# Kernel tuning notes

Hardware: AMD Instinct MI355X
Metric: run time of the kernel (lower is better)

## Reference

```python
import jax, jax.numpy as jnp
import numpy as np
import math

D = 768
H = 12
DFF = 3072
HD = D // H


def _layernorm(x, g, b, eps=1e-5):
    mu = jnp.mean(x, axis=-1, keepdims=True)
    var = jnp.var(x, axis=-1, keepdims=True)
    return (x - mu) * jax.lax.rsqrt(var + eps) * g + b


def setup_inputs() -> dict:
    key = jax.random.key(0)
    ks = jax.random.split(key, 12)
    B, S = 2, 4096
    s = 1.0 / math.sqrt(D)
    sf = 1.0 / math.sqrt(DFF)
    return {
        "x": jax.random.normal(ks[0], (B, S, D), jnp.float32),
        "attention_mask": jnp.ones((B, S), jnp.int32),
        "ln1_g": jnp.ones((D,), jnp.float32),
        "ln1_b": jnp.zeros((D,), jnp.float32),
        "ln2_g": jnp.ones((D,), jnp.float32),
        "ln2_b": jnp.zeros((D,), jnp.float32),
        "Wq": jax.random.normal(ks[1], (D, D), jnp.float32) * s,
        "bq": jnp.zeros((D,), jnp.float32),
        "Wk": jax.random.normal(ks[2], (D, D), jnp.float32) * s,
        "bk": jnp.zeros((D,), jnp.float32),
        "Wv": jax.random.normal(ks[3], (D, D), jnp.float32) * s,
        "bv": jnp.zeros((D,), jnp.float32),
        "Wo": jax.random.normal(ks[4], (D, D), jnp.float32) * s,
        "bo": jnp.zeros((D,), jnp.float32),
        "W1": jax.random.normal(ks[5], (D, DFF), jnp.float32) * s,
        "b1": jnp.zeros((DFF,), jnp.float32),
        "W2": jax.random.normal(ks[6], (DFF, D), jnp.float32) * sf,
        "b2": jnp.zeros((D,), jnp.float32),
    }


def _block(x, attention_mask, ln1_g, ln1_b, ln2_g, ln2_b,
           Wq, bq, Wk, bk, Wv, bv, Wo, bo, W1, b1, W2, b2):
    B, S, _ = x.shape
    h = _layernorm(x, ln1_g, ln1_b)
    q = (h @ Wq + bq).reshape(B, S, H, HD)
    k = (h @ Wk + bk).reshape(B, S, H, HD)
    v = (h @ Wv + bv).reshape(B, S, H, HD)
    # scores: [B, H, S, S]
    dots = jnp.einsum('bqhd,bkhd->bhqk', q, k) / math.sqrt(HD)
    causal = jnp.tril(jnp.ones((S, S), bool))  # True = keep
    keep = causal[None, None] & (attention_mask != 0)[:, None, None, :]
    dots = jnp.where(keep, dots, -jnp.inf)
    probs = jax.nn.softmax(dots, axis=-1)
    ctx = jnp.einsum('bhqk,bkhd->bqhd', probs, v).reshape(B, S, D)
    sa = ctx @ Wo + bo  # dropout = identity (eval)
    x = x + sa
    h2 = _layernorm(x, ln2_g, ln2_b)
    ff = jax.nn.relu(h2 @ W1 + b1) @ W2 + b2
    return x + ff


def reference(x, attention_mask, ln1_g, ln1_b, ln2_g, ln2_b,
              Wq, bq, Wk, bk, Wv, bv, Wo, bo, W1, b1, W2, b2):
    return _block(x, attention_mask, ln1_g, ln1_b, ln2_g, ln2_b,
                  Wq, bq, Wk, bk, Wv, bv, Wo, bo, W1, b1, W2, b2)
```

## Files before the change

### kernel.cpp

```cpp
#include <hip/hip_runtime.h>
#include <hip/hip_bf16.h>
#include <math.h>

#define S_LEN 4096
#define DMODEL 768
#define NHEAD 12
#define HDIM 64
#define DFF_ 3072
#define MROWS 8192

typedef __bf16 bf16;
typedef __bf16 bf16x4 __attribute__((ext_vector_type(4)));
typedef __bf16 bf16x8 __attribute__((ext_vector_type(8)));
typedef float f32x4 __attribute__((ext_vector_type(4)));

union F4 { float4 v; float f[4]; };
union U2 { bf16 h[2]; unsigned u; };
union U8 { unsigned u[4]; bf16x8 v; };

__device__ __forceinline__ void gld_lds16(void* lds, const void* g) {
    __builtin_amdgcn_global_load_lds(
        (const __attribute__((address_space(1))) unsigned int*)g,
        (__attribute__((address_space(3))) unsigned int*)lds, 16, 0, 0);
}

template<typename OUT>
__global__ __launch_bounds__(256) void ln_kernel(const float* __restrict__ x,
                                                 const float* __restrict__ g,
                                                 const float* __restrict__ bta,
                                                 OUT* __restrict__ out) {
    const int row = blockIdx.x;
    const int t = threadIdx.x;
    const float* xr = x + (size_t)row * DMODEL;
    float v0 = xr[t], v1 = xr[t + 256], v2 = xr[t + 512];
    float s = v0 + v1 + v2;
    float ss = v0 * v0 + v1 * v1 + v2 * v2;
    for (int o = 32; o > 0; o >>= 1) {
        s += __shfl_down(s, o, 64);
        ss += __shfl_down(ss, o, 64);
    }
    __shared__ float sm[4], sm2[4];
    const int w = t >> 6, lane = t & 63;
    if (lane == 0) { sm[w] = s; sm2[w] = ss; }
    __syncthreads();
    s = sm[0] + sm[1] + sm[2] + sm[3];
    ss = sm2[0] + sm2[1] + sm2[2] + sm2[3];
    const float mu = s * (1.0f / DMODEL);
    const float var = ss * (1.0f / DMODEL) - mu * mu;
    const float rs = rsqrtf(var + 1e-5f);
    OUT* orow = out + (size_t)row * DMODEL;
    orow[t]       = (OUT)((v0 - mu) * rs * g[t]       + bta[t]);
    orow[t + 256] = (OUT)((v1 - mu) * rs * g[t + 256] + bta[t + 256]);
    orow[t + 512] = (OUT)((v2 - mu) * rs * g[t + 512] + bta[t + 512]);
}

__global__ __launch_bounds__(256) void wtrans_kernel(const float* __restrict__ W,
                                                     bf16* __restrict__ Wt,
                                                     int K, int N) {
    __shared__ float tile[64][65];
    const int tid = threadIdx.x;
    const int n0 = blockIdx.x * 64, k0 = blockIdx.y * 64;
    const int lr = tid >> 4, lc = (tid & 15) << 2;
#pragma unroll
    for (int i = 0; i < 4; ++i) {
        const int r = lr + i * 16;
        F4 w; w.v = *(const float4*)&W[(size_t)(k0 + r) * N + n0 + lc];
#pragma unroll
        for (int j = 0; j < 4; ++j) tile[r][lc + j] = w.f[j];
    }
    __syncthreads();
#pragma unroll
    for (int i = 0; i < 4; ++i) {
        const int n = lr + i * 16;
        bf16x4 o;
#pragma unroll
        for (int j = 0; j < 4; ++j) o[j] = (bf16)tile[lc + j][n];
        *(bf16x4*)&Wt[(size_t)(n0 + n) * K + k0 + lc] = o;
    }
}

template<bool RELU, bool RES, bool OUT_BF16>
__global__ __launch_bounds__(256) void mgemm_kernel(
    const bf16* __restrict__ A,
    const bf16* __restrict__ Wt0, const float* __restrict__ bias0, void* __restrict__ C0,
    const bf16* __restrict__ Wt1, const float* __restrict__ bias1, void* __restrict__ C1,
    const bf16* __restrict__ Wt2, const float* __restrict__ bias2, void* __restrict__ C2,
    const float* __restrict__ R, int M, int N, int K,
    float sc0, float sc1, float sc2) {
    const bf16* Wt = Wt0; const float* bias = bias0; void* C = C0; float sc = sc0;
    if (blockIdx.z == 1) { Wt = Wt1; bias = bias1; C = C1; sc = sc1; }
    if (blockIdx.z == 2) { Wt = Wt2; bias = bias2; C = C2; sc = sc2; }

    __shared__ bf16 As[128 * 32];
    __shared__ bf16 Bs[128 * 32];

    const int tid = threadIdx.x;
    const int wave = tid >> 6, lane = tid & 63;
    const int row0 = blockIdx.y * 128, col0 = blockIdx.x * 128;
    const int wr = (wave >> 1) * 64, wc = (wave & 1) * 64;
    const int mrow = lane & 15, kq = (lane >> 4) * 8;

    const int st_row = (lane >> 2);
    const int st_off = (lane & 3) * 16;

    f32x4 acc[4][4] = {};

    const char* Ab = (const char*)(A + (size_t)row0 * K);
    const char* Bb = (const char*)(Wt + (size_t)col0 * K);
    const size_t strideA = (size_t)K * 2;

    for (int k0 = 0; k0 < K; k0 += 32) {
#pragma unroll
        for (int issue = 0; issue < 2; ++issue) {
            const int r = wave * 32 + issue * 16 + st_row;
            gld_lds16((char*)As + (wave * 32 + issue * 16) * 64,
                      Ab + (size_t)r * strideA + k0 * 2 + st_off);
            gld_lds16((char*)Bs + (wave * 32 + issue * 16) * 64,
                      Bb + (size_t)r * strideA + k0 * 2 + st_off);
        }
        __syncthreads();
        bf16x8 af[4], bfr[4];
#pragma unroll
        for (int mi = 0; mi < 4; ++mi)
            af[mi] = *(const bf16x8*)&As[(wr + mi * 16 + mrow) * 32 + kq];
#pragma unroll
        for (int ni = 0; ni < 4; ++ni)
            bfr[ni] = *(const bf16x8*)&Bs[(wc + ni * 16 + mrow) * 32 + kq];
#pragma unroll
        for (int mi = 0; mi < 4; ++mi)
#pragma unroll
            for (int ni = 0; ni < 4; ++ni)
                acc[mi][ni] = __builtin_amdgcn_mfma_f32_16x16x32_bf16(
                    af[mi], bfr[ni], acc[mi][ni], 0, 0, 0);
        __syncthreads();
    }

    const int quad = lane >> 4;
    float bv[4];
#pragma unroll
    for (int ni = 0; ni < 4; ++ni) bv[ni] = bias[col0 + wc + ni * 16 + mrow];
#pragma unroll
    for (int mi = 0; mi < 4; ++mi) {
#pragma unroll
        for (int r = 0; r < 4; ++r) {
            const int row = row0 + wr + mi * 16 + quad * 4 + r;
#pragma unroll
            for (int ni = 0; ni < 4; ++ni) {
                const int col = col0 + wc + ni * 16 + mrow;
                float v = acc[mi][ni][r] + bv[ni];
                if (RES) v += R[(size_t)row * N + col];
                v *= sc;
                if (RELU) v = fmaxf(v, 0.0f);
                if (OUT_BF16) ((bf16*)C)[(size_t)row * N + col] = (bf16)v;
                else          ((float*)C)[(size_t)row * N + col] = v;
            }
        }
    }
}

__global__ __launch_bounds__(256) void mattn_kernel(
    const bf16* __restrict__ Q, const bf16* __restrict__ K,
    const bf16* __restrict__ V, const int* __restrict__ amask,
    bf16* __restrict__ O) {
    const int bx = blockIdx.x, h = blockIdx.y, b = blockIdx.z;

    __shared__ bf16 Ks[64][72];
    __shared__ bf16 Vt[64][72];
    __shared__ bf16 Os[64][72];
    __shared__ float mk[64];
    __shared__ int flagv;

    const int tid = threadIdx.x;
    const int wave = tid >> 6, lane = tid & 63;
    const int l = lane & 15, quad = lane >> 4;
    const int qh = quad >> 1;
    const int srcA = (quad & 1) * 32 + l;
    const int srcB = srcA + 16;
    const float NEG_INF = -__builtin_huge_valf();

    const int kr = tid >> 2, ks = (tid & 3) * 16;
    const int vk0 = (tid & 31) * 2, vds = (tid >> 5) * 8;

#pragma unroll 1
    for (int pass = 0; pass < 2; ++pass) {
        const int qt = pass ? bx : (63 - bx);

        const bf16* Qb = Q + (size_t)(b * S_LEN + qt * 64 + wave * 16 + l) * DMODEL + h * HDIM;
        const bf16x8 qf0 = *(const bf16x8*)(Qb + quad * 8);
        const bf16x8 qf1 = *(const bf16x8*)(Qb + 32 + quad * 8);

        float m_run = NEG_INF, l_run = 0.0f;
        f32x4 acc[4] = {};

        for (int kt = 0; kt <= qt; ++kt) {
            __syncthreads();
            {
                const bf16* kg = K + (size_t)(b * S_LEN + kt * 64 + kr) * DMODEL + h * HDIM + ks;
                *(bf16x8*)&Ks[kr][ks]     = *(const bf16x8*)kg;
                *(bf16x8*)&Ks[kr][ks + 8] = *(const bf16x8*)(kg + 8);
            }
            {
                const bf16* vg = V + (size_t)(b * S_LEN + kt * 64 + vk0) * DMODEL + h * HDIM + vds;
                bf16x8 v0 = *(const bf16x8*)vg;
                bf16x8 v1 = *(const bf16x8*)(vg + DMODEL);
#pragma unroll
                for (int i = 0; i < 8; ++i) {
                    U2 w; w.h[0] = v0[i]; w.h[1] = v1[i];
                    *(unsigned*)&Vt[vds + i][vk0] = w.u;
                }
            }
            if (wave == 0) {
                const int mv = amask[b * S_LEN + kt * 64 + lane];
                mk[lane] = mv ? 0.0f : NEG_INF;
                unsigned long long bal = __ballot(mv != 0);
                if (lane == 0) flagv = (bal == ~0ULL);
            }
            __syncthreads();
            const int allv = flagv;

            f32x4 sreg[4] = {};
#pragma unroll
            for (int mi = 0; mi < 4; ++mi) {
                bf16x8 kf0 = *(const bf16x8*)&Ks[mi * 16 + l][quad * 8];
                bf16x8 kf1 = *(const bf16x8*)&Ks[mi * 16 + l][32 + quad * 8];
                sreg[mi] = __builtin_amdgcn_mfma_f32_16x16x32_bf16(kf0, qf0, sreg[mi], 0, 0, 0);
                sreg[mi] = __builtin_amdgcn_mfma_f32_16x16x32_bf16(kf1, qf1, sreg[mi], 0, 0, 0);
            }
            if (!allv) {
#pragma unroll
                for (int mi = 0; mi < 4; ++mi) {
                    F4 m4; m4.v = *(const float4*)&mk[mi * 16 + quad * 4];
#pragma unroll
                    for (int r = 0; r < 4; ++r) sreg[mi][r] += m4.f[r];
                }
            }
            if (kt == qt) {
#pragma unroll
                for (int mi = 0; mi < 4; ++mi)
#pragma unroll
                    for (int r = 0; r < 4; ++r)
                        if (mi * 16 + quad * 4 + r > wave * 16 + l)
                            sreg[mi][r] = NEG_INF;
            }

            float mloc = sreg[0][0];
#pragma unroll
            for (int mi = 0; mi < 4; ++mi)
#pragma unroll
                for (int r = 0; r < 4; ++r) mloc = fmaxf(mloc, sreg[mi][r]);
            mloc = fmaxf(mloc, __shfl_xor(mloc, 16, 64));
            mloc = fmaxf(mloc, __shfl_xor(mloc, 32, 64));
            const float mn = fmaxf(m_run, mloc);
            const float alpha = __builtin_amdgcn_exp2f(m_run - mn);
            m_run = mn;
            float ls = 0.0f;
#pragma unroll
            for (int mi = 0; mi < 4; ++mi)
#pragma unroll
                for (int r = 0; r < 4; ++r) {
                    const float p = __builtin_amdgcn_exp2f(sreg[mi][r] - mn);
                    sreg[mi][r] = p;
                    ls += p;
                }
            ls += __shfl_xor(ls, 16, 64);
            ls += __shfl_xor(ls, 32, 64);
            l_run = l_run * alpha + ls;
#pragma unroll
            for (int mi = 0; mi < 4; ++mi)
#pragma unroll
                for (int r = 0; r < 4; ++r) acc[mi][r] *= alpha;

            unsigned pk[4][2];
#pragma unroll
            for (int mi = 0; mi < 4; ++mi) {
                U2 w0; w0.h[0] = (bf16)sreg[mi][0]; w0.h[1] = (bf16)sreg[mi][1];
                U2 w1; w1.h[0] = (bf16)sreg[mi][2]; w1.h[1] = (bf16)sreg[mi][3];
                pk[mi][0] = w0.u; pk[mi][1] = w1.u;
            }
            bf16x8 pfrag[2];
#pragma unroll
            for (int kc = 0; kc < 2; ++kc) {
                U8 u;
#pragma unroll
                for (int t = 0; t < 2; ++t) {
                    const unsigned a0 = (unsigned)__shfl((int)pk[2 * kc][t],     srcA, 64);
                    const unsigned b0 = (unsigned)__shfl((int)pk[2 * kc + 1][t], srcA, 64);
                    u.u[t] = qh ? b0 : a0;
                    const unsigned a1 = (unsigned)__shfl((int)pk[2 * kc][t],     srcB, 64);
                    const unsigned b1 = (unsigned)__shfl((int)pk[2 * kc + 1][t], srcB, 64);
                    u.u[2 + t] = qh ? b1 : a1;
                }
                pfrag[kc] = u.v;
            }
#pragma unroll
            for (int mi = 0; mi < 4; ++mi) {
                bf16x8 vf0 = *(const bf16x8*)&Vt[mi * 16 + l][quad * 8];
                bf16x8 vf1 = *(const bf16x8*)&Vt[mi * 16 + l][32 + quad * 8];
                acc[mi] = __builtin_amdgcn_mfma_f32_16x16x32_bf16(vf0, pfrag[0], acc[mi], 0, 0, 0);
                acc[mi] = __builtin_amdgcn_mfma_f32_16x16x32_bf16(vf1, pfrag[1], acc[mi], 0, 0, 0);
            }
        }

        const float rinv = 1.0f / l_run;
#pragma unroll
        for (int mi = 0; mi < 4; ++mi) {
            U2 w0; w0.h[0] = (bf16)(acc[mi][0] * rinv); w0.h[1] = (bf16)(acc[mi][1] * rinv);
            U2 w1; w1.h[0] = (bf16)(acc[mi][2] * rinv); w1.h[1] = (bf16)(acc[mi][3] * rinv);
            *(unsigned*)&Os[wave * 16 + l][mi * 16 + quad * 4]     = w0.u;
            *(unsigned*)&Os[wave * 16 + l][mi * 16 + quad * 4 + 2] = w1.u;
        }
        __syncthreads();
        {
            const int orow = tid >> 2, oseg = (tid & 3) * 16;
            bf16* Og = O + (size_t)(b * S_LEN + qt * 64 + orow) * DMODEL + h * HDIM + oseg;
            *(bf16x8*)Og       = *(const bf16x8*)&Os[orow][oseg];
            *(bf16x8*)(Og + 8) = *(const bf16x8*)&Os[orow][oseg + 8];
        }
    }
}

extern "C" void kernel_launch(void* const* d_in, const int* in_sizes, int n_in,
                              void* d_out, int out_size, void* d_ws, size_t ws_size,
                              hipStream_t stream) {
    const float* x     = (const float*)d_in[0];
    const int*   amask = (const int*)  d_in[1];
    const float* ln1_g = (const float*)d_in[2];
    const float* ln1_b = (const float*)d_in[3];
    const float* ln2_g = (const float*)d_in[4];
    const float* ln2_b = (const float*)d_in[5];
    const float* Wq = (const float*)d_in[6];  const float* bq = (const float*)d_in[7];
    const float* Wk = (const float*)d_in[8];  const float* bk = (const float*)d_in[9];
    const float* Wv = (const float*)d_in[10]; const float* bv = (const float*)d_in[11];
    const float* Wo = (const float*)d_in[12]; const float* bo = (const float*)d_in[13];
    const float* W1 = (const float*)d_in[14]; const float* b1 = (const float*)d_in[15];
    const float* W2 = (const float*)d_in[16]; const float* b2 = (const float*)d_in[17];
    float* out = (float*)d_out;

    char* ws = (char*)d_ws;
    const size_t WSML = (size_t)DMODEL * DMODEL * 2;
    const size_t WBIG = (size_t)DMODEL * DFF_ * 2;
    bf16* Wqt = (bf16*)(ws + 0 * WSML);
    bf16* Wkt = (bf16*)(ws + 1 * WSML);
    bf16* Wvt = (bf16*)(ws + 2 * WSML);
    bf16* Wot = (bf16*)(ws + 3 * WSML);
    bf16* W1t = (bf16*)(ws + 4 * WSML);
    bf16* W2t = (bf16*)(ws + 4 * WSML + WBIG);
    char* act = ws + 4 * WSML + 2 * WBIG;

    const size_t HB = (size_t)MROWS * DMODEL * 2;
    const size_t FB = (size_t)MROWS * DMODEL * 4;
    bf16*  h    = (bf16*)(act);
    bf16*  qb   = (bf16*)(act + HB);
    bf16*  kb   = (bf16*)(act + 2 * HB);
    bf16*  vb   = (bf16*)(act + 3 * HB);
    bf16*  ctx  = h;
    float* x1   = (float*)(act + 4 * HB);
    bf16*  f    = (bf16*)(act + 4 * HB + FB);
    bf16*  h2   = h;

    const float SCL = 0.125f * 1.44269504089f;

    wtrans_kernel<<<dim3(DMODEL / 64, DMODEL / 64), 256, 0, stream>>>(Wq, Wqt, DMODEL, DMODEL);
    wtrans_kernel<<<dim3(DMODEL / 64, DMODEL / 64), 256, 0, stream>>>(Wk, Wkt, DMODEL, DMODEL);
    wtrans_kernel<<<dim3(DMODEL / 64, DMODEL / 64), 256, 0, stream>>>(Wv, Wvt, DMODEL, DMODEL);
    wtrans_kernel<<<dim3(DMODEL / 64, DMODEL / 64), 256, 0, stream>>>(Wo, Wot, DMODEL, DMODEL);
    wtrans_kernel<<<dim3(DFF_ / 64, DMODEL / 64), 256, 0, stream>>>(W1, W1t, DMODEL, DFF_);
    wtrans_kernel<<<dim3(DMODEL / 64, DFF_ / 64), 256, 0, stream>>>(W2, W2t, DFF_, DMODEL);

    ln_kernel<bf16><<<MROWS, 256, 0, stream>>>(x, ln1_g, ln1_b, h);
    mgemm_kernel<false, false, true><<<dim3(DMODEL / 128, MROWS / 128, 3), 256, 0, stream>>>(
        h, Wqt, bq, qb, Wkt, bk, kb, Wvt, bv, vb, nullptr, MROWS, DMODEL, DMODEL,
        SCL, 1.0f, 1.0f);
    mattn_kernel<<<dim3(32, NHEAD, 2), 256, 0, stream>>>(qb, kb, vb, amask, ctx);
    mgemm_kernel<false, true, false><<<dim3(DMODEL / 128, MROWS / 128, 1), 256, 0, stream>>>(
        ctx, Wot, bo, x1, Wot, bo, x1, Wot, bo, x1, x, MROWS, DMODEL, DMODEL,
        1.0f, 1.0f, 1.0f);
    ln_kernel<bf16><<<MROWS, 256, 0, stream>>>(x1, ln2_g, ln2_b, h2);
    mgemm_kernel<true, false, true><<<dim3(DFF_ / 128, MROWS / 128, 1), 256, 0, stream>>>(
        h2, W1t, b1, f, W1t, b1, f, W1t, b1, f, nullptr, MROWS, DFF_, DMODEL,
        1.0f, 1.0f, 1.0f);
    mgemm_kernel<false, true, false><<<dim3(DMODEL / 128, MROWS / 128, 1), 256, 0, stream>>>(
        f, W2t, b2, out, W2t, b2, out, W2t, b2, out, x1, MROWS, DMODEL, DFF_,
        1.0f, 1.0f, 1.0f);
}
```

Before: 515.0 us.

## Use 64-row GEMM tiles for N=768 GEMMs and one query tile per attention block

The GEMM kernel gains an MT template parameter. The output-projection and FFN-down GEMMs (N=768) now use 64x128 tiles, which doubles their block count and should fill the GPU better. The attention kernel drops its paired-pass scheme and gives each block a single query tile over a 64-wide grid, heaviest tiles first, so there are more blocks to schedule. LDS padding shrinks from 72 to 68 columns, which can change bank-conflict behaviour. The trade-off is lower per-block reuse of the B tiles in the smaller GEMMs and possibly worse load balance in attention.

```diff
diff --git a/kernel.cpp b/kernel.cpp
--- a/kernel.cpp
+++ b/kernel.cpp
@@ -79,7 +79,7 @@
     }
 }
 
-template<bool RELU, bool RES, bool OUT_BF16>
+template<int MT, bool RELU, bool RES, bool OUT_BF16>
 __global__ __launch_bounds__(256) void mgemm_kernel(
     const bf16* __restrict__ A,
     const bf16* __restrict__ Wt0, const float* __restrict__ bias0, void* __restrict__ C0,
@@ -91,61 +91,73 @@
     if (blockIdx.z == 1) { Wt = Wt1; bias = bias1; C = C1; sc = sc1; }
     if (blockIdx.z == 2) { Wt = Wt2; bias = bias2; C = C2; sc = sc2; }
 
-    __shared__ bf16 As[128 * 32];
+    constexpr int NI = (MT == 128) ? 4 : 2;
+    __shared__ bf16 As[MT * 32];
     __shared__ bf16 Bs[128 * 32];
 
     const int tid = threadIdx.x;
     const int wave = tid >> 6, lane = tid & 63;
-    const int row0 = blockIdx.y * 128, col0 = blockIdx.x * 128;
-    const int wr = (wave >> 1) * 64, wc = (wave & 1) * 64;
+    const int row0 = blockIdx.y * MT, col0 = blockIdx.x * 128;
+    const int wr = (MT == 128) ? (wave >> 1) * 64 : 0;
+    const int wc = (MT == 128) ? (wave & 1) * 64 : wave * 32;
     const int mrow = lane & 15, kq = (lane >> 4) * 8;
 
     const int st_row = (lane >> 2);
     const int st_off = (lane & 3) * 16;
 
-    f32x4 acc[4][4] = {};
+    f32x4 acc[4][NI] = {};
 
     const char* Ab = (const char*)(A + (size_t)row0 * K);
     const char* Bb = (const char*)(Wt + (size_t)col0 * K);
     const size_t strideA = (size_t)K * 2;
 
     for (int k0 = 0; k0 < K; k0 += 32) {
+        if (MT == 128) {
+#pragma unroll
+            for (int issue = 0; issue < 2; ++issue) {
+                const int r = wave * 32 + issue * 16 + st_row;
+                gld_lds16((char*)As + (wave * 32 + issue * 16) * 64,
+                          Ab + (size_t)r * strideA + k0 * 2 + st_off);
+            }
+        } else {
+            const int r = wave * 16 + st_row;
+            gld_lds16((char*)As + (wave * 16) * 64,
+                      Ab + (size_t)r * strideA + k0 * 2 + st_off);
+        }
 #pragma unroll
         for (int issue = 0; issue < 2; ++issue) {
             const int r = wave * 32 + issue * 16 + st_row;
-            gld_lds16((char*)As + (wave * 32 + issue * 16) * 64,
-                      Ab + (size_t)r * strideA + k0 * 2 + st_off);
             gld_lds16((char*)Bs + (wave * 32 + issue * 16) * 64,
                       Bb + (size_t)r * strideA + k0 * 2 + st_off);
         }
         __syncthreads();
-        bf16x8 af[4], bfr[4];
+        bf16x8 af[4], bfr[NI];
 #pragma unroll
         for (int mi = 0; mi < 4; ++mi)
             af[mi] = *(const bf16x8*)&As[(wr + mi * 16 + mrow) * 32 + kq];
 #pragma unroll
-        for (int ni = 0; ni < 4; ++ni)
+        for (int ni = 0; ni < NI; ++ni)
             bfr[ni] = *(const bf16x8*)&Bs[(wc + ni * 16 + mrow) * 32 + kq];
 #pragma unroll
         for (int mi = 0; mi < 4; ++mi)
 #pragma unroll
-            for (int ni = 0; ni < 4; ++ni)
+            for (int ni = 0; ni < NI; ++ni)
                 acc[mi][ni] = __builtin_amdgcn_mfma_f32_16x16x32_bf16(
                     af[mi], bfr[ni], acc[mi][ni], 0, 0, 0);
         __syncthreads();
     }
 
     const int quad = lane >> 4;
-    float bv[4];
-#pragma unroll
-    for (int ni = 0; ni < 4; ++ni) bv[ni] = bias[col0 + wc + ni * 16 + mrow];
+    float bv[NI];
+#pragma unroll
+    for (int ni = 0; ni < NI; ++ni) bv[ni] = bias[col0 + wc + ni * 16 + mrow];
 #pragma unroll
     for (int mi = 0; mi < 4; ++mi) {
 #pragma unroll
         for (int r = 0; r < 4; ++r) {
             const int row = row0 + wr + mi * 16 + quad * 4 + r;
 #pragma unroll
-            for (int ni = 0; ni < 4; ++ni) {
+            for (int ni = 0; ni < NI; ++ni) {
                 const int col = col0 + wc + ni * 16 + mrow;
                 float v = acc[mi][ni][r] + bv[ni];
                 if (RES) v += R[(size_t)row * N + col];
@@ -162,11 +174,12 @@
     const bf16* __restrict__ Q, const bf16* __restrict__ K,
     const bf16* __restrict__ V, const int* __restrict__ amask,
     bf16* __restrict__ O) {
-    const int bx = blockIdx.x, h = blockIdx.y, b = blockIdx.z;
-
-    __shared__ bf16 Ks[64][72];
-    __shared__ bf16 Vt[64][72];
-    __shared__ bf16 Os[64][72];
+    const int qt = 63 - blockIdx.x;
+    const int h = blockIdx.y, b = blockIdx.z;
+
+    __shared__ bf16 Ks[64][68];
+    __shared__ bf16 Vt[64][68];
+    __shared__ bf16 Os[64][68];
     __shared__ float mk[64];
     __shared__ int flagv;
 
@@ -181,141 +194,136 @@
     const int kr = tid >> 2, ks = (tid & 3) * 16;
     const int vk0 = (tid & 31) * 2, vds = (tid >> 5) * 8;
 
-#pragma unroll 1
-    for (int pass = 0; pass < 2; ++pass) {
-        const int qt = pass ? bx : (63 - bx);
-
-        const bf16* Qb = Q + (size_t)(b * S_LEN + qt * 64 + wave * 16 + l) * DMODEL + h * HDIM;
-        const bf16x8 qf0 = *(const bf16x8*)(Qb + quad * 8);
-        const bf16x8 qf1 = *(const bf16x8*)(Qb + 32 + quad * 8);
-
-        float m_run = NEG_INF, l_run = 0.0f;
-        f32x4 acc[4] = {};
-
-        for (int kt = 0; kt <= qt; ++kt) {
-            __syncthreads();
-            {
-                const bf16* kg = K + (size_t)(b * S_LEN + kt * 64 + kr) * DMODEL + h * HDIM + ks;
-                *(bf16x8*)&Ks[kr][ks]     = *(const bf16x8*)kg;
-                *(bf16x8*)&Ks[kr][ks + 8] = *(const bf16x8*)(kg + 8);
-            }
-            {
-                const bf16* vg = V + (size_t)(b * S_LEN + kt * 64 + vk0) * DMODEL + h * HDIM + vds;
-                bf16x8 v0 = *(const bf16x8*)vg;
-                bf16x8 v1 = *(const bf16x8*)(vg + DMODEL);
-#pragma unroll
-                for (int i = 0; i < 8; ++i) {
-                    U2 w; w.h[0] = v0[i]; w.h[1] = v1[i];
-                    *(unsigned*)&Vt[vds + i][vk0] = w.u;
-                }
-            }
-            if (wave == 0) {
-                const int mv = amask[b * S_LEN + kt * 64 + lane];
-                mk[lane] = mv ? 0.0f : NEG_INF;
-                unsigned long long bal = __ballot(mv != 0);
-                if (lane == 0) flagv = (bal == ~0ULL);
-            }
-            __syncthreads();
-            const int allv = flagv;
-
-            f32x4 sreg[4] = {};
-#pragma unroll
-            for (int mi = 0; mi < 4; ++mi) {
-                bf16x8 kf0 = *(const bf16x8*)&Ks[mi * 16 + l][quad * 8];
-                bf16x8 kf1 = *(const bf16x8*)&Ks[mi * 16 + l][32 + quad * 8];
-                sreg[mi] = __builtin_amdgcn_mfma_f32_16x16x32_bf16(kf0, qf0, sreg[mi], 0, 0, 0);
-                sreg[mi] = __builtin_amdgcn_mfma_f32_16x16x32_bf16(kf1, qf1, sreg[mi], 0, 0, 0);
-            }
-            if (!allv) {
-#pragma unroll
-                for (int mi = 0; mi < 4; ++mi) {
-                    F4 m4; m4.v = *(const float4*)&mk[mi * 16 + quad * 4];
-#pragma unroll
-                    for (int r = 0; r < 4; ++r) sreg[mi][r] += m4.f[r];
-                }
-            }
-            if (kt == qt) {
-#pragma unroll
-                for (int mi = 0; mi < 4; ++mi)
-#pragma unroll
-                    for (int r = 0; r < 4; ++r)
-                        if (mi * 16 + quad * 4 + r > wave * 16 + l)
-                            sreg[mi][r] = NEG_INF;
-            }
-
-            float mloc = sreg[0][0];
-#pragma unroll
-            for (int mi = 0; mi < 4; ++mi)
-#pragma unroll
-                for (int r = 0; r < 4; ++r) mloc = fmaxf(mloc, sreg[mi][r]);
-            mloc = fmaxf(mloc, __shfl_xor(mloc, 16, 64));
-            mloc = fmaxf(mloc, __shfl_xor(mloc, 32, 64));
-            const float mn = fmaxf(m_run, mloc);
-            const float alpha = __builtin_amdgcn_exp2f(m_run - mn);
-            m_run = mn;
-            float ls = 0.0f;
-#pragma unroll
-            for (int mi = 0; mi < 4; ++mi)
-#pragma unroll
-                for (int r = 0; r < 4; ++r) {
-                    const float p = __builtin_amdgcn_exp2f(sreg[mi][r] - mn);
-                    sreg[mi][r] = p;
-                    ls += p;
-                }
-            ls += __shfl_xor(ls, 16, 64);
-            ls += __shfl_xor(ls, 32, 64);
-            l_run = l_run * alpha + ls;
-#pragma unroll
-            for (int mi = 0; mi < 4; ++mi)
-#pragma unroll
-                for (int r = 0; r < 4; ++r) acc[mi][r] *= alpha;
-
-            unsigned pk[4][2];
-#pragma unroll
-            for (int mi = 0; mi < 4; ++mi) {
-                U2 w0; w0.h[0] = (bf16)sreg[mi][0]; w0.h[1] = (bf16)sreg[mi][1];
-                U2 w1; w1.h[0] = (bf16)sreg[mi][2]; w1.h[1] = (bf16)sreg[mi][3];
-                pk[mi][0] = w0.u; pk[mi][1] = w1.u;
-            }
-            bf16x8 pfrag[2];
-#pragma unroll
-            for (int kc = 0; kc < 2; ++kc) {
-                U8 u;
-#pragma unroll
-                for (int t = 0; t < 2; ++t) {
-                    const unsigned a0 = (unsigned)__shfl((int)pk[2 * kc][t],     srcA, 64);
-                    const unsigned b0 = (unsigned)__shfl((int)pk[2 * kc + 1][t], srcA, 64);
-                    u.u[t] = qh ? b0 : a0;
-                    const unsigned a1 = (unsigned)__shfl((int)pk[2 * kc][t],     srcB, 64);
-                    const unsigned b1 = (unsigned)__shfl((int)pk[2 * kc + 1][t], srcB, 64);
-                    u.u[2 + t] = qh ? b1 : a1;
-                }
-                pfrag[kc] = u.v;
-            }
-#pragma unroll
-            for (int mi = 0; mi < 4; ++mi) {
-                bf16x8 vf0 = *(const bf16x8*)&Vt[mi * 16 + l][quad * 8];
-                bf16x8 vf1 = *(const bf16x8*)&Vt[mi * 16 + l][32 + quad * 8];
-                acc[mi] = __builtin_amdgcn_mfma_f32_16x16x32_bf16(vf0, pfrag[0], acc[mi], 0, 0, 0);
-                acc[mi] = __builtin_amdgcn_mfma_f32_16x16x32_bf16(vf1, pfrag[1], acc[mi], 0, 0, 0);
-            }
-        }
-
-        const float rinv = 1.0f / l_run;
-#pragma unroll
-        for (int mi = 0; mi < 4; ++mi) {
-            U2 w0; w0.h[0] = (bf16)(acc[mi][0] * rinv); w0.h[1] = (bf16)(acc[mi][1] * rinv);
-            U2 w1; w1.h[0] = (bf16)(acc[mi][2] * rinv); w1.h[1] = (bf16)(acc[mi][3] * rinv);
-            *(unsigned*)&Os[wave * 16 + l][mi * 16 + quad * 4]     = w0.u;
-            *(unsigned*)&Os[wave * 16 + l][mi * 16 + quad * 4 + 2] = w1.u;
-        }
+    const bf16* Qb = Q + (size_t)(b * S_LEN + qt * 64 + wave * 16 + l) * DMODEL + h * HDIM;
+    const bf16x8 qf0 = *(const bf16x8*)(Qb + quad * 8);
+    const bf16x8 qf1 = *(const bf16x8*)(Qb + 32 + quad * 8);
+
+    float m_run = NEG_INF, l_run = 0.0f;
+    f32x4 acc[4] = {};
+
+    for (int kt = 0; kt <= qt; ++kt) {
         __syncthreads();
         {
-            const int orow = tid >> 2, oseg = (tid & 3) * 16;
-            bf16* Og = O + (size_t)(b * S_LEN + qt * 64 + orow) * DMODEL + h * HDIM + oseg;
-            *(bf16x8*)Og       = *(const bf16x8*)&Os[orow][oseg];
-            *(bf16x8*)(Og + 8) = *(const bf16x8*)&Os[orow][oseg + 8];
-        }
+            const bf16* kg = K + (size_t)(b * S_LEN + kt * 64 + kr) * DMODEL + h * HDIM + ks;
+            *(bf16x8*)&Ks[kr][ks]     = *(const bf16x8*)kg;
+            *(bf16x8*)&Ks[kr][ks + 8] = *(const bf16x8*)(kg + 8);
+        }
+        {
+            const bf16* vg = V + (size_t)(b * S_LEN + kt * 64 + vk0) * DMODEL + h * HDIM + vds;
+            bf16x8 v0 = *(const bf16x8*)vg;
+            bf16x8 v1 = *(const bf16x8*)(vg + DMODEL);
+#pragma unroll
+            for (int i = 0; i < 8; ++i) {
+                U2 w; w.h[0] = v0[i]; w.h[1] = v1[i];
+                *(unsigned*)&Vt[vds + i][vk0] = w.u;
+            }
+        }
+        if (wave == 0) {
+            const int mv = amask[b * S_LEN + kt * 64 + lane];
+            mk[lane] = mv ? 0.0f : NEG_INF;
+            unsigned long long bal = __ballot(mv != 0);
+            if (lane == 0) flagv = (bal == ~0ULL);
+        }
+        __syncthreads();
+        const int allv = flagv;
+
+        f32x4 sreg[4] = {};
+#pragma unroll
+        for (int mi = 0; mi < 4; ++mi) {
+            bf16x8 kf0 = *(const bf16x8*)&Ks[mi * 16 + l][quad * 8];
+            bf16x8 kf1 = *(const bf16x8*)&Ks[mi * 16 + l][32 + quad * 8];
+            sreg[mi] = __builtin_amdgcn_mfma_f32_16x16x32_bf16(kf0, qf0, sreg[mi], 0, 0, 0);
+            sreg[mi] = __builtin_amdgcn_mfma_f32_16x16x32_bf16(kf1, qf1, sreg[mi], 0, 0, 0);
+        }
+        if (!allv) {
+#pragma unroll
+            for (int mi = 0; mi < 4; ++mi) {
+                F4 m4; m4.v = *(const float4*)&mk[mi * 16 + quad * 4];
+#pragma unroll
+                for (int r = 0; r < 4; ++r) sreg[mi][r] += m4.f[r];
+            }
+        }
+        if (kt == qt) {
+#pragma unroll
+            for (int mi = 0; mi < 4; ++mi)
+#pragma unroll
+                for (int r = 0; r < 4; ++r)
+                    if (mi * 16 + quad * 4 + r > wave * 16 + l)
+                        sreg[mi][r] = NEG_INF;
+        }
+
+        float mloc = sreg[0][0];
+#pragma unroll
+        for (int mi = 0; mi < 4; ++mi)
+#pragma unroll
+            for (int r = 0; r < 4; ++r) mloc = fmaxf(mloc, sreg[mi][r]);
+        mloc = fmaxf(mloc, __shfl_xor(mloc, 16, 64));
+        mloc = fmaxf(mloc, __shfl_xor(mloc, 32, 64));
+        const float mn = fmaxf(m_run, mloc);
+        const float alpha = __builtin_amdgcn_exp2f(m_run - mn);
+        m_run = mn;
+        float ls = 0.0f;
+#pragma unroll
+        for (int mi = 0; mi < 4; ++mi)
+#pragma unroll
+            for (int r = 0; r < 4; ++r) {
+                const float p = __builtin_amdgcn_exp2f(sreg[mi][r] - mn);
+                sreg[mi][r] = p;
+                ls += p;
+            }
+        ls += __shfl_xor(ls, 16, 64);
+        ls += __shfl_xor(ls, 32, 64);
+        l_run = l_run * alpha + ls;
+#pragma unroll
+        for (int mi = 0; mi < 4; ++mi)
+#pragma unroll
+            for (int r = 0; r < 4; ++r) acc[mi][r] *= alpha;
+
+        unsigned pk[4][2];
+#pragma unroll
+        for (int mi = 0; mi < 4; ++mi) {
+            U2 w0; w0.h[0] = (bf16)sreg[mi][0]; w0.h[1] = (bf16)sreg[mi][1];
+            U2 w1; w1.h[0] = (bf16)sreg[mi][2]; w1.h[1] = (bf16)sreg[mi][3];
+            pk[mi][0] = w0.u; pk[mi][1] = w1.u;
+        }
+        bf16x8 pfrag[2];
+#pragma unroll
+        for (int kc = 0; kc < 2; ++kc) {
+            U8 u;
+#pragma unroll
+            for (int t = 0; t < 2; ++t) {
+                const unsigned a0 = (unsigned)__shfl((int)pk[2 * kc][t],     srcA, 64);
+                const unsigned b0 = (unsigned)__shfl((int)pk[2 * kc + 1][t], srcA, 64);
+                u.u[t] = qh ? b0 : a0;
+                const unsigned a1 = (unsigned)__shfl((int)pk[2 * kc][t],     srcB, 64);
+                const unsigned b1 = (unsigned)__shfl((int)pk[2 * kc + 1][t], srcB, 64);
+                u.u[2 + t] = qh ? b1 : a1;
+            }
+            pfrag[kc] = u.v;
+        }
+#pragma unroll
+        for (int mi = 0; mi < 4; ++mi) {
+            bf16x8 vf0 = *(const bf16x8*)&Vt[mi * 16 + l][quad * 8];
+            bf16x8 vf1 = *(const bf16x8*)&Vt[mi * 16 + l][32 + quad * 8];
+            acc[mi] = __builtin_amdgcn_mfma_f32_16x16x32_bf16(vf0, pfrag[0], acc[mi], 0, 0, 0);
+            acc[mi] = __builtin_amdgcn_mfma_f32_16x16x32_bf16(vf1, pfrag[1], acc[mi], 0, 0, 0);
+        }
+    }
+
+    const float rinv = 1.0f / l_run;
+#pragma unroll
+    for (int mi = 0; mi < 4; ++mi) {
+        U2 w0; w0.h[0] = (bf16)(acc[mi][0] * rinv); w0.h[1] = (bf16)(acc[mi][1] * rinv);
+        U2 w1; w1.h[0] = (bf16)(acc[mi][2] * rinv); w1.h[1] = (bf16)(acc[mi][3] * rinv);
+        *(unsigned*)&Os[wave * 16 + l][mi * 16 + quad * 4]     = w0.u;
+        *(unsigned*)&Os[wave * 16 + l][mi * 16 + quad * 4 + 2] = w1.u;
+    }
+    __syncthreads();
+    {
+        const int orow = tid >> 2, oseg = (tid & 3) * 16;
+        bf16* Og = O + (size_t)(b * S_LEN + qt * 64 + orow) * DMODEL + h * HDIM + oseg;
+        *(bf16x8*)Og       = *(const bf16x8*)&Os[orow][oseg];
+        *(bf16x8*)(Og + 8) = *(const bf16x8*)&Os[orow][oseg + 8];
     }
 }
 
@@ -368,18 +376,18 @@
     wtrans_kernel<<<dim3(DMODEL / 64, DFF_ / 64), 256, 0, stream>>>(W2, W2t, DFF_, DMODEL);
 
     ln_kernel<bf16><<<MROWS, 256, 0, stream>>>(x, ln1_g, ln1_b, h);
-    mgemm_kernel<false, false, true><<<dim3(DMODEL / 128, MROWS / 128, 3), 256, 0, stream>>>(
+    mgemm_kernel<128, false, false, true><<<dim3(DMODEL / 128, MROWS / 128, 3), 256, 0, stream>>>(
         h, Wqt, bq, qb, Wkt, bk, kb, Wvt, bv, vb, nullptr, MROWS, DMODEL, DMODEL,
         SCL, 1.0f, 1.0f);
-    mattn_kernel<<<dim3(32, NHEAD, 2), 256, 0, stream>>>(qb, kb, vb, amask, ctx);
-    mgemm_kernel<false, true, false><<<dim3(DMODEL / 128, MROWS / 128, 1), 256, 0, stream>>>(
+    mattn_kernel<<<dim3(64, NHEAD, 2), 256, 0, stream>>>(qb, kb, vb, amask, ctx);
+    mgemm_kernel<64, false, true, false><<<dim3(DMODEL / 128, MROWS / 64, 1), 256, 0, stream>>>(
         ctx, Wot, bo, x1, Wot, bo, x1, Wot, bo, x1, x, MROWS, DMODEL, DMODEL,
         1.0f, 1.0f, 1.0f);
     ln_kernel<bf16><<<MROWS, 256, 0, stream>>>(x1, ln2_g, ln2_b, h2);
-    mgemm_kernel<true, false, true><<<dim3(DFF_ / 128, MROWS / 128, 1), 256, 0, stream>>>(
+    mgemm_kernel<128, true, false, true><<<dim3(DFF_ / 128, MROWS / 128, 1), 256, 0, stream>>>(
         h2, W1t, b1, f, W1t, b1, f, W1t, b1, f, nullptr, MROWS, DFF_, DMODEL,
         1.0f, 1.0f, 1.0f);
-    mgemm_kernel<false, true, false><<<dim3(DMODEL / 128, MROWS / 128, 1), 256, 0, stream>>>(
+    mgemm_kernel<64, false, true, false><<<dim3(DMODEL / 128, MROWS / 64, 1), 256, 0, stream>>>(
         f, W2t, b2, out, W2t, b2, out, W2t, b2, out, x1, MROWS, DMODEL, DFF_,
         1.0f, 1.0f, 1.0f);
 }
```

Result: slower. 603.9 us (+17.3%).
